# Optimization experiments

Hardware: AMD Instinct MI355X
Metric: run time of the kernel (lower is better)

## Reference

```python
import jax, jax.numpy as jnp
import numpy as np
import math

B, T, C = 2, 1024, 1024
NEMBD = 1024
NATTN = 1024
NHEAD = 16
CTX = 1024
HS = NATTN // NHEAD          # head size = 64
ROT = HS // 2                # rotary dims = 32


def rotate_half(x):
    x1, x2 = x[..., : x.shape[-1] // 2], x[..., x.shape[-1] // 2 :]
    return jnp.concatenate((-x2, x1), axis=-1)


def setup_inputs() -> dict:
    key = jax.random.key(0)
    ks = jax.random.split(key, 16)
    s = 0.02
    inp = {
        "x": jax.random.normal(ks[0], (B, T, C), dtype=jnp.float32),
        # time-decay params (torch inits them to ones; add noise for a nontrivial test)
        "time_w": 1.0 + s * jax.random.normal(ks[1], (NHEAD, CTX), dtype=jnp.float32),
        "time_alpha": 1.0 + s * jax.random.normal(ks[2], (NHEAD, 1, CTX), dtype=jnp.float32),
        "time_beta": 1.0 + s * jax.random.normal(ks[3], (NHEAD, CTX, 1), dtype=jnp.float32),
        "time_gamma": 1.0 + s * jax.random.normal(ks[4], (CTX, 1), dtype=jnp.float32),
        # projections (stored as (in, out) for x @ W)
        "Wq": s * jax.random.normal(ks[5], (NEMBD, NATTN), dtype=jnp.float32),
        "bq": s * jax.random.normal(ks[6], (NATTN,), dtype=jnp.float32),
        "Wk": s * jax.random.normal(ks[7], (NEMBD, NATTN), dtype=jnp.float32),
        "bk": s * jax.random.normal(ks[8], (NATTN,), dtype=jnp.float32),
        "Wv": s * jax.random.normal(ks[9], (NEMBD, NATTN), dtype=jnp.float32),
        "bv": s * jax.random.normal(ks[10], (NATTN,), dtype=jnp.float32),
        # 1x1 conv over head channels: (out_head, in_head)
        "Wmix": s * jax.random.normal(ks[11], (NHEAD, NHEAD), dtype=jnp.float32),
        "Wo": s * jax.random.normal(ks[12], (NATTN, NEMBD), dtype=jnp.float32),
        "bo": s * jax.random.normal(ks[13], (NEMBD,), dtype=jnp.float32),
    }
    return inp


def reference(x, time_w, time_alpha, time_beta, time_gamma,
              Wq, bq, Wk, bk, Wv, bv, Wmix, Wo, bo):
    Bx, Tx, Cx = x.shape
    TT = CTX

    # --- relative time-decay weight matrix (H, T, T) ---
    w = jnp.pad(time_w, ((0, 0), (0, TT)))          # (H, 2TT)
    w = jnp.tile(w, (1, TT))                        # (H, 2TT*TT)
    w = w[:, :-TT].reshape(NHEAD, TT, 2 * TT - 1)
    w = w[:, :, TT - 1:]                            # (H, TT, TT)
    w = w[:, :Tx, :Tx] * time_alpha[:, :, :Tx] * time_beta[:, :Tx, :]

    # --- time shift of the first half of channels ---
    half = Cx // 2
    x_shift = jnp.pad(x[:, :, :half], ((0, 0), (1, 0), (0, 0)))[:, :Tx, :]
    xs = jnp.concatenate([x_shift, x[:, :, half:]], axis=-1)

    # --- q/k/v projections -> (B, H, T, hs) ---
    q = (xs @ Wq + bq).reshape(Bx, Tx, NHEAD, HS).transpose(0, 2, 1, 3)
    k = (xs @ Wk + bk).reshape(Bx, Tx, NHEAD, HS).transpose(0, 2, 1, 3)
    v = (xs @ Wv + bv).reshape(Bx, Tx, NHEAD, HS).transpose(0, 2, 1, 3)

    # --- rotary on the first ROT dims of each head (base = ctx_len) ---
    qr, q_pass = q[..., :ROT], q[..., ROT:]
    kr, k_pass = k[..., :ROT], k[..., ROT:]
    inv_freq = 1.0 / (jnp.float32(CTX) ** (jnp.arange(0, ROT, 2, dtype=jnp.float32) / ROT))
    t = jnp.arange(Tx, dtype=jnp.float32)
    freqs = t[:, None] * inv_freq[None, :]          # (T, ROT/2)
    emb = jnp.concatenate((freqs, freqs), axis=-1)  # (T, ROT)
    cos, sin = jnp.cos(emb), jnp.sin(emb)
    qr = qr * cos + rotate_half(qr) * sin
    kr = kr * cos + rotate_half(kr) * sin
    q = jnp.concatenate((qr, q_pass), axis=-1)
    k = jnp.concatenate((kr, k_pass), axis=-1)

    # --- attention with time decay and cross-head 1x1 mix ---
    att = jnp.einsum('bhtd,bhsd->bhts', q, k) * (1.0 / math.sqrt(HS))
    att = jax.nn.softmax(att, axis=-1)
    att = att * w[None]                              # (B,H,T,T) * (1,H,T,T)
    att = jnp.einsum('gh,bhts->bgts', Wmix, att)     # 1x1 conv over head channel
    y = jnp.einsum('bhts,bhsd->bhtd', att, v)
    y = y.transpose(0, 2, 1, 3).reshape(Bx, Tx, NATTN)
    return (y @ Wo + bo) * time_gamma[:Tx, :]
```

## Files before the change

### kernel.cpp

```cpp
#include <hip/hip_runtime.h>

typedef unsigned short u16;
typedef unsigned int u32;
typedef __attribute__((ext_vector_type(8))) short bf16x8;
typedef __attribute__((ext_vector_type(4))) float f32x4;

#define MFMA(a,b,c) __builtin_amdgcn_mfma_f32_16x16x32_bf16(a,b,c,0,0,0)

__device__ __forceinline__ float b2f(u16 u){
  union { unsigned int i; float f; } v; v.i = ((unsigned int)u)<<16; return v.f;
}
__device__ __forceinline__ u16 f2b(float f){
  union { float f; unsigned int i; } v; v.f = f;
  unsigned int r = (v.i + 0x7FFFu + ((v.i>>16)&1u))>>16;
  return (u16)r;
}
__device__ __forceinline__ void gld16(const u16* g, u16* l){
  __builtin_amdgcn_global_load_lds((const __attribute__((address_space(1))) u32*)g,
                                   (__attribute__((address_space(3))) u32*)l, 16, 0, 0);
}

__global__ __launch_bounds__(256) void k_pre(
    const float* __restrict__ x,
    const float* __restrict__ Wq, const float* __restrict__ Wk,
    const float* __restrict__ Wv, const float* __restrict__ Wo,
    u16* __restrict__ xs, u16* __restrict__ WT, u16* __restrict__ WoT)
{
  int bid = blockIdx.x;
  int tid = threadIdx.x;
  if (bid < 1024){
    int idx = bid*256 + tid;
    size_t e = (size_t)idx*8;
    int c = (int)(e & 1023);
    int t = (int)((e>>10)&1023);
    float4 f0 = {0.f,0.f,0.f,0.f}, f1 = {0.f,0.f,0.f,0.f};
    const float* src = nullptr;
    if (c < 512){ if (t > 0) src = x + e - 1024; }
    else        { src = x + e; }
    if (src){ f0 = *(const float4*)src; f1 = *(const float4*)(src+4); }
    u16 o[8];
    o[0]=f2b(f0.x); o[1]=f2b(f0.y); o[2]=f2b(f0.z); o[3]=f2b(f0.w);
    o[4]=f2b(f1.x); o[5]=f2b(f1.y); o[6]=f2b(f1.z); o[7]=f2b(f1.w);
    *(uint4*)(xs + e) = *(const uint4*)o;
    return;
  }
  int z  = (bid-1024)>>8;
  int rc = (bid-1024)&255;
  const float* src = (z==0)?Wq:((z==1)?Wk:((z==2)?Wv:Wo));
  u16* dst = (z==3)? WoT : (WT + (size_t)z*1048576);
  int c0 = (rc&15)*64, r0 = (rc>>4)*64;
  __shared__ u16 tile[64][72];
  int r = tid>>2, cc = (tid&3)*16;
  const float* sp = src + (size_t)(r0+r)*1024 + c0+cc;
  float4 a0 = *(const float4*)(sp);
  float4 a1 = *(const float4*)(sp+4);
  float4 a2 = *(const float4*)(sp+8);
  float4 a3 = *(const float4*)(sp+12);
  tile[r][cc+0]=f2b(a0.x); tile[r][cc+1]=f2b(a0.y); tile[r][cc+2]=f2b(a0.z); tile[r][cc+3]=f2b(a0.w);
  tile[r][cc+4]=f2b(a1.x); tile[r][cc+5]=f2b(a1.y); tile[r][cc+6]=f2b(a1.z); tile[r][cc+7]=f2b(a1.w);
  tile[r][cc+8]=f2b(a2.x); tile[r][cc+9]=f2b(a2.y); tile[r][cc+10]=f2b(a2.z); tile[r][cc+11]=f2b(a2.w);
  tile[r][cc+12]=f2b(a3.x); tile[r][cc+13]=f2b(a3.y); tile[r][cc+14]=f2b(a3.z); tile[r][cc+15]=f2b(a3.w);
  __syncthreads();
  int c = tid>>2, rr = (tid&3)*16;
  uint4 o0,o1; u16* p0=(u16*)&o0; u16* p1=(u16*)&o1;
  #pragma unroll
  for (int i=0;i<8;i++){ p0[i]=tile[rr+i][c]; p1[i]=tile[rr+8+i][c]; }
  *(uint4*)(dst + (size_t)(c0+c)*1024 + r0+rr)   = o0;
  *(uint4*)(dst + (size_t)(c0+c)*1024 + r0+rr+8) = o1;
}

__global__ __launch_bounds__(256) void k_gemm_qkv(
    const u16* __restrict__ A, const u16* __restrict__ Bt,
    const float* __restrict__ bq, const float* __restrict__ bk, const float* __restrict__ bv,
    u16* __restrict__ qb, u16* __restrict__ kb, u16* __restrict__ vT)
{
  __shared__ u16 As[128*32];
  __shared__ u16 Bs[64*32];
  const int n0 = blockIdx.x*64, m0 = blockIdx.y*128;
  const int tid = threadIdx.x, lane = tid&63, wave = tid>>6;
  const int quad = lane>>4, l16 = lane&15;
  const int wm = (wave>>1)*64, wn = (wave&1)*32;
  f32x4 zero = {0.f,0.f,0.f,0.f};
  f32x4 acc[4][2];
  #pragma unroll
  for (int i=0;i<4;i++){ acc[i][0]=zero; acc[i][1]=zero; }
  const int srow = (lane>>2), scol = (lane&3)*8;
  const u16* pa0 = A  + (size_t)(m0 + wave*16 + srow)*1024 + scol;
  const u16* pb0 = Bt + (size_t)(n0 + wave*16 + srow)*1024 + scol;
  u16* lA0 = &As[(wave*16)*32];
  u16* lA1 = &As[(64 + wave*16)*32];
  u16* lB0 = &Bs[(wave*16)*32];
  for (int k0=0;k0<1024;k0+=32){
    __syncthreads();
    gld16(pa0 + k0,           lA0);
    gld16(pa0 + 64*1024 + k0, lA1);
    gld16(pb0 + k0,           lB0);
    __syncthreads();
    bf16x8 af[4], bfr[2];
    #pragma unroll
    for (int mt=0;mt<4;mt++) af[mt]  = *(const bf16x8*)&As[(wm+mt*16+l16)*32 + quad*8];
    #pragma unroll
    for (int nt=0;nt<2;nt++) bfr[nt] = *(const bf16x8*)&Bs[(wn+nt*16+l16)*32 + quad*8];
    #pragma unroll
    for (int mt=0;mt<4;mt++){
      acc[mt][0] = MFMA(af[mt], bfr[0], acc[mt][0]);
      acc[mt][1] = MFMA(af[mt], bfr[1], acc[mt][1]);
    }
  }
  const int which = n0>>10;
  const int nn0 = (n0 & 1023) + wn;
  const int h = (n0 & 1023)>>6;
  const float* barr = (which==0)?bq:((which==1)?bk:bv);
  float bias0 = barr[nn0 + l16];
  float bias1 = barr[nn0 + 16 + l16];
  if (which == 2){
    #pragma unroll
    for (int mt=0;mt<4;mt++)
      #pragma unroll
      for (int r=0;r<4;r++){
        int m = m0 + wm + mt*16 + quad*4 + r;
        int bb = m>>10, t = m&1023;
        size_t base = (size_t)(bb*16+h)*65536 + t;
        int d0 = wn + l16;
        vT[base + (size_t)d0*1024]      = f2b(acc[mt][0][r] + bias0);
        vT[base + (size_t)(d0+16)*1024] = f2b(acc[mt][1][r] + bias1);
      }
  } else {
    const float scale = (which==0)?0.125f:1.0f;
    u16* dst = (which==0)? qb : kb;
    if (wn == 0){
      const float e = exp2f(-0.625f*(float)l16);
      #pragma unroll
      for (int mt=0;mt<4;mt++)
        #pragma unroll
        for (int r=0;r<4;r++){
          int m = m0 + wm + mt*16 + quad*4 + r;
          int bb = m>>10, t = m&1023;
          float f = (float)t * e;
          float cs = cosf(f), sn = sinf(f);
          float x0 = acc[mt][0][r] + bias0;
          float x1 = acc[mt][1][r] + bias1;
          float v0 = (x0*cs - x1*sn)*scale;
          float v1 = (x1*cs + x0*sn)*scale;
          size_t ob = (((size_t)(bb*16+h))*1024 + (size_t)t)*64 + l16;
          dst[ob]    = f2b(v0);
          dst[ob+16] = f2b(v1);
        }
    } else {
      #pragma unroll
      for (int mt=0;mt<4;mt++)
        #pragma unroll
        for (int r=0;r<4;r++){
          int m = m0 + wm + mt*16 + quad*4 + r;
          int bb = m>>10, t = m&1023;
          float v2 = (acc[mt][0][r] + bias0)*scale;
          float v3 = (acc[mt][1][r] + bias1)*scale;
          size_t ob = (((size_t)(bb*16+h))*1024 + (size_t)t)*64 + 32 + l16;
          dst[ob]    = f2b(v2);
          dst[ob+16] = f2b(v3);
        }
    }
  }
}

__global__ __launch_bounds__(256) void k_gemm_out(
    const u16* __restrict__ A, const u16* __restrict__ Bt,
    const float* __restrict__ bo, const float* __restrict__ gamma, float* __restrict__ out)
{
  __shared__ u16 As[64*32];
  __shared__ u16 Bs[64*32];
  const int n0 = blockIdx.x*64, m0 = blockIdx.y*64;
  const int tid = threadIdx.x, lane = tid&63, wave = tid>>6;
  const int quad = lane>>4, l16 = lane&15;
  const int wm = (wave>>1)*32, wn = (wave&1)*32;
  f32x4 zero = {0.f,0.f,0.f,0.f};
  f32x4 acc[2][2];
  #pragma unroll
  for (int i=0;i<2;i++){ acc[i][0]=zero; acc[i][1]=zero; }
  const int srow = (lane>>2), scol = (lane&3)*8;
  const u16* pa0 = A  + (size_t)(m0 + wave*16 + srow)*1024 + scol;
  const u16* pb0 = Bt + (size_t)(n0 + wave*16 + srow)*1024 + scol;
  u16* lA0 = &As[(wave*16)*32];
  u16* lB0 = &Bs[(wave*16)*32];
  for (int k0=0;k0<1024;k0+=32){
    __syncthreads();
    gld16(pa0 + k0, lA0);
    gld16(pb0 + k0, lB0);
    __syncthreads();
    bf16x8 af[2], bfr[2];
    #pragma unroll
    for (int mt=0;mt<2;mt++) af[mt]  = *(const bf16x8*)&As[(wm+mt*16+l16)*32 + quad*8];
    #pragma unroll
    for (int nt=0;nt<2;nt++) bfr[nt] = *(const bf16x8*)&Bs[(wn+nt*16+l16)*32 + quad*8];
    #pragma unroll
    for (int mt=0;mt<2;mt++){
      acc[mt][0] = MFMA(af[mt], bfr[0], acc[mt][0]);
      acc[mt][1] = MFMA(af[mt], bfr[1], acc[mt][1]);
    }
  }
  #pragma unroll
  for (int nt=0;nt<2;nt++){
    int colg = n0 + wn + nt*16 + l16;
    float bias = bo[colg];
    #pragma unroll
    for (int mt=0;mt<2;mt++)
      #pragma unroll
      for (int r=0;r<4;r++){
        int m = m0 + wm + mt*16 + quad*4 + r;
        int t = m&1023;
        float val = (acc[mt][nt][r] + bias)*gamma[t];
        out[(size_t)m*1024 + colg] = val;
      }
  }
}

__global__ __launch_bounds__(1024) void k_sm(
    const u16* __restrict__ q, const u16* __restrict__ k,
    const float* __restrict__ tw, const float* __restrict__ alpha, const float* __restrict__ beta,
    u16* __restrict__ P)
{
  const int tb = blockIdx.x, h = blockIdx.y, b = blockIdx.z;
  const int t0b = tb*64;
  const int tid = threadIdx.x;
  const int wave = tid>>6, lane = tid&63, quad = lane>>4, l16 = lane&15;
  const int wt = wave>>2, ws = wave&3;

  __shared__ u16 qs[64*76];
  __shared__ u16 ks[256*76];
  __shared__ float tws[1024];
  __shared__ float als[1024];
  __shared__ float pm[4][64];
  __shared__ float pl[4][64];
  __shared__ float fm[64];
  __shared__ float fr[64];

  const size_t bh = (size_t)(b*16+h)*65536;
  const u16* qp = q + bh;
  const u16* kp = k + bh;

  if (tid < 512){
    int row = tid>>3, g = tid&7;
    *(uint4*)&qs[row*76 + g*8] = *(const uint4*)(qp + (size_t)(t0b+row)*64 + g*8);
  }
  tws[tid] = tw[h*1024 + tid];
  als[tid] = alpha[h*1024 + tid];
  __syncthreads();

  bf16x8 qf0 = *(const bf16x8*)&qs[(wt*16+l16)*76 + quad*8];
  bf16x8 qf1 = *(const bf16x8*)&qs[(wt*16+l16)*76 + quad*8 + 32];

  f32x4 acc[16];
  #pragma unroll
  for (int i=0;i<16;i++){ acc[i][0]=0.f; acc[i][1]=0.f; acc[i][2]=0.f; acc[i][3]=0.f; }

  #pragma unroll
  for (int c=0;c<4;c++){
    if (c) __syncthreads();
    {
      int row = tid>>3, g = tid&7;
      *(uint4*)&ks[row*76 + g*8]       = *(const uint4*)(kp + (size_t)(c*256+row)*64 + g*8);
      *(uint4*)&ks[(row+128)*76 + g*8] = *(const uint4*)(kp + (size_t)(c*256+row+128)*64 + g*8);
    }
    __syncthreads();
    #pragma unroll
    for (int j=0;j<4;j++){
      int lt = j*4 + ws;
      bf16x8 kf0 = *(const bf16x8*)&ks[(lt*16+l16)*76 + quad*8];
      bf16x8 kf1 = *(const bf16x8*)&ks[(lt*16+l16)*76 + quad*8 + 32];
      acc[c*4+j] = MFMA(qf0, kf0, acc[c*4+j]);
      acc[c*4+j] = MFMA(qf1, kf1, acc[c*4+j]);
    }
  }

  float mrow[4], lrow[4];
  #pragma unroll
  for (int r=0;r<4;r++){
    float m = acc[0][r];
    #pragma unroll
    for (int a=1;a<16;a++) m = fmaxf(m, acc[a][r]);
    #pragma unroll
    for (int off=1; off<16; off<<=1) m = fmaxf(m, __shfl_xor(m, off));
    float l = 0.f;
    #pragma unroll
    for (int a=0;a<16;a++) l += __expf(acc[a][r]-m);
    #pragma unroll
    for (int off=1; off<16; off<<=1) l += __shfl_xor(l, off);
    mrow[r]=m; lrow[r]=l;
  }
  if (l16==0){
    #pragma unroll
    for (int r=0;r<4;r++){
      pm[ws][wt*16+quad*4+r] = mrow[r];
      pl[ws][wt*16+quad*4+r] = lrow[r];
    }
  }
  __syncthreads();
  if (tid < 64){
    float m0s = pm[0][tid], m1s = pm[1][tid], m2s = pm[2][tid], m3s = pm[3][tid];
    float m = fmaxf(fmaxf(m0s,m1s), fmaxf(m2s,m3s));
    float l = pl[0][tid]*__expf(m0s-m) + pl[1][tid]*__expf(m1s-m)
            + pl[2][tid]*__expf(m2s-m) + pl[3][tid]*__expf(m3s-m);
    fm[tid] = m;
    fr[tid] = beta[h*1024 + t0b + tid] / l;
  }
  __syncthreads();

  u16* Pp = P + (((size_t)b)<<24) + (((size_t)h)<<10);
  float m_f[4], r_f[4]; int trow[4];
  #pragma unroll
  for (int r=0;r<4;r++){
    int rg = wt*16+quad*4+r;
    m_f[r] = fm[rg]; r_f[r] = fr[rg]; trow[r] = t0b + rg;
  }
  const int slim = tb*4 + wt;
  #pragma unroll
  for (int c=0;c<4;c++)
    #pragma unroll
    for (int j=0;j<4;j++){
      int st = c*16 + j*4 + ws;
      if (st > slim) continue;
      int s = st*16 + l16;
      float av = als[s];
      #pragma unroll
      for (int r=0;r<4;r++){
        int t = trow[r];
        float p = 0.f;
        if (s <= t)
          p = __expf(acc[c*4+j][r]-m_f[r])*r_f[r]*tws[1023+s-t]*av;
        Pp[((size_t)t<<14) + s] = f2b(p);
      }
    }
}

__global__ __launch_bounds__(256) void k_mix(const u16* __restrict__ P, const float* __restrict__ Wm,
                                             u16* __restrict__ Ab)
{
  const int t = blockIdx.x, b = blockIdx.y;
  const int tid = threadIdx.x;
  const int g = tid>>4, sg = tid&15;
  __shared__ u16 Ps[16*264];
  float w[16];
  #pragma unroll
  for (int h=0;h<16;h++) w[h] = Wm[g*16+h];
  const int tmaxr = t|15;
  const int ncw = (t>>8) + 1;
  const size_t slab = (((size_t)b)<<24) + (((size_t)t)<<14);
  const u16* pp = P + slab;
  u16* ap = Ab + slab;
  for (int c=0;c<ncw;c++){
    int s0 = c*256;
    if (c) __syncthreads();
    int colg = sg*16;
    uint4 z = {0u,0u,0u,0u};
    uint4 v0 = z, v1 = z;
    if (s0+colg <= tmaxr){
      v0 = *(const uint4*)(pp + ((size_t)g<<10) + s0+colg);
      v1 = *(const uint4*)(pp + ((size_t)g<<10) + s0+colg+8);
    }
    *(uint4*)&Ps[g*264+colg]   = v0;
    *(uint4*)&Ps[g*264+colg+8] = v1;
    __syncthreads();
    if (s0 + sg*16 > tmaxr) continue;
    float acc[16];
    #pragma unroll
    for (int i=0;i<16;i++) acc[i]=0.f;
    #pragma unroll
    for (int h=0;h<16;h++){
      float wh = w[h];
      #pragma unroll
      for (int j=0;j<4;j++){
        ushort4 u = *(const ushort4*)&Ps[h*264 + sg*16 + j*4];
        acc[j*4+0] += wh*b2f(u.x);
        acc[j*4+1] += wh*b2f(u.y);
        acc[j*4+2] += wh*b2f(u.z);
        acc[j*4+3] += wh*b2f(u.w);
      }
    }
    u16 o[16];
    #pragma unroll
    for (int i=0;i<16;i++) o[i] = f2b(acc[i]);
    *(uint4*)(ap + ((size_t)g<<10) + s0 + sg*16)     = *(uint4*)&o[0];
    *(uint4*)(ap + ((size_t)g<<10) + s0 + sg*16 + 8) = *(uint4*)&o[8];
  }
}

__global__ __launch_bounds__(1024) void k_pv(const u16* __restrict__ Ab, const u16* __restrict__ vT,
                                             u16* __restrict__ y)
{
  const int tb = blockIdx.x;
  const int bg = blockIdx.y;
  const int b = bg>>4, g = bg&15;
  const int t0b = tb*64;
  const int tid = threadIdx.x;
  const int wave = tid>>6, lane = tid&63, quad = lane>>4, l16 = lane&15;
  const int wt = wave>>2, wd = wave&3;
  __shared__ u16 As[64*264];
  __shared__ u16 Vs[64*264];
  const u16* ap = Ab + (((size_t)b)<<24) + ((size_t)g<<10);
  const u16* vp = vT + (size_t)bg*65536;
  f32x4 acc = {0.f,0.f,0.f,0.f};
  const int nc = tb/4 + 1;
  const int row = tid>>4, col = (tid&15)*16;
  const int trow_g = t0b + row;
  const int tmax = trow_g|15;
  for (int c=0;c<nc;c++){
    if (c) __syncthreads();
    int s0 = c*256;
    uint4 z = {0u,0u,0u,0u};
    uint4 a0 = z, a1 = z;
    if (s0 + col <= tmax){
      a0 = *(const uint4*)(ap + ((size_t)trow_g<<14) + s0+col);
      a1 = *(const uint4*)(ap + ((size_t)trow_g<<14) + s0+col+8);
    }
    *(uint4*)&As[row*264+col]   = a0;
    *(uint4*)&As[row*264+col+8] = a1;
    *(uint4*)&Vs[row*264+col]   = *(const uint4*)(vp + (size_t)row*1024 + s0+col);
    *(uint4*)&Vs[row*264+col+8] = *(const uint4*)(vp + (size_t)row*1024 + s0+col+8);
    __syncthreads();
    #pragma unroll
    for (int ks=0;ks<8;ks++){
      bf16x8 af  = *(const bf16x8*)&As[(wt*16+l16)*264 + ks*32 + quad*8];
      bf16x8 bfv = *(const bf16x8*)&Vs[(wd*16+l16)*264 + ks*32 + quad*8];
      acc = MFMA(af, bfv, acc);
    }
  }
  #pragma unroll
  for (int r=0;r<4;r++){
    int t = t0b + wt*16 + quad*4 + r;
    y[(size_t)(b*1024+t)*1024 + g*64 + wd*16 + l16] = f2b(acc[r]);
  }
}

__global__ void k_fail(float* out){ if (threadIdx.x==0) out[0] = 1e30f; }

extern "C" void kernel_launch(void* const* d_in, const int* in_sizes, int n_in,
                              void* d_out, int out_size, void* d_ws, size_t ws_size,
                              hipStream_t stream)
{
  const float* x     = (const float*)d_in[0];
  const float* tw    = (const float*)d_in[1];
  const float* alpha = (const float*)d_in[2];
  const float* beta  = (const float*)d_in[3];
  const float* gamma = (const float*)d_in[4];
  const float* Wq    = (const float*)d_in[5];
  const float* bq    = (const float*)d_in[6];
  const float* Wk    = (const float*)d_in[7];
  const float* bk    = (const float*)d_in[8];
  const float* Wv    = (const float*)d_in[9];
  const float* bv    = (const float*)d_in[10];
  const float* Wmix  = (const float*)d_in[11];
  const float* Wo    = (const float*)d_in[12];
  const float* bo    = (const float*)d_in[13];
  float* out = (float*)d_out;

  char* ws = (char*)d_ws;
  size_t off = 0;
  auto take = [&](size_t bytes)->char*{
    char* p = ws + off; off += (bytes + 255) & ~(size_t)255; return p;
  };
  u16*   xs  = (u16*)take((size_t)2097152*2);
  u16*   WT  = (u16*)take((size_t)3145728*2);
  u16*   WoT = (u16*)take((size_t)1048576*2);
  u16*   qb  = (u16*)take((size_t)2097152*2);
  u16*   kb  = (u16*)take((size_t)2097152*2);
  u16*   vTb = (u16*)take((size_t)2097152*2);
  u16*   yb  = (u16*)take((size_t)2097152*2);
  u16*   P   = (u16*)take((size_t)33554432*2);
  u16*   A   = (u16*)take((size_t)33554432*2);
  if (off > ws_size){
    hipLaunchKernelGGL(k_fail, dim3(1), dim3(64), 0, stream, out);
    return;
  }

  hipLaunchKernelGGL(k_pre, dim3(2048), dim3(256), 0, stream,
                     x, Wq, Wk, Wv, Wo, xs, WT, WoT);
  hipLaunchKernelGGL(k_gemm_qkv, dim3(48,16), dim3(256), 0, stream,
                     xs, WT, bq, bk, bv, qb, kb, vTb);
  hipLaunchKernelGGL(k_sm, dim3(16,16,2), dim3(1024), 0, stream,
                     qb, kb, tw, alpha, beta, P);
  hipLaunchKernelGGL(k_mix, dim3(1024,2), dim3(256), 0, stream, P, Wmix, A);
  hipLaunchKernelGGL(k_pv, dim3(16,32), dim3(1024), 0, stream, A, vTb, yb);
  hipLaunchKernelGGL(k_gemm_out, dim3(16,32), dim3(256), 0, stream, yb, WoT, bo, gamma, out);
}
```

Before: 208.3 us.

## Fuse cross-head mix into PV kernel and drop the intermediate mixed-attention buffer

Removes the separate k_mix kernel and the 64MB intermediate A buffer. The new k_mpv kernel computes the 16-head mix for each row chunk while staging the attention tile into LDS, then runs the PV MFMA loop as before. This eliminates a full write and re-read of the mixed attention matrix and one launch. The cost is that each output-head block now re-reads all 16 heads of P, so global or L2 read traffic for P rises up to 16x. The grid is reordered so that the 16 head blocks sharing a time tile are adjacent, which is meant to let those repeated reads hit in cache.

```diff
diff --git a/kernel.cpp b/kernel.cpp
--- a/kernel.cpp
+++ b/kernel.cpp
@@ -332,63 +332,11 @@
     }
 }
 
-__global__ __launch_bounds__(256) void k_mix(const u16* __restrict__ P, const float* __restrict__ Wm,
-                                             u16* __restrict__ Ab)
-{
-  const int t = blockIdx.x, b = blockIdx.y;
-  const int tid = threadIdx.x;
-  const int g = tid>>4, sg = tid&15;
-  __shared__ u16 Ps[16*264];
-  float w[16];
-  #pragma unroll
-  for (int h=0;h<16;h++) w[h] = Wm[g*16+h];
-  const int tmaxr = t|15;
-  const int ncw = (t>>8) + 1;
-  const size_t slab = (((size_t)b)<<24) + (((size_t)t)<<14);
-  const u16* pp = P + slab;
-  u16* ap = Ab + slab;
-  for (int c=0;c<ncw;c++){
-    int s0 = c*256;
-    if (c) __syncthreads();
-    int colg = sg*16;
-    uint4 z = {0u,0u,0u,0u};
-    uint4 v0 = z, v1 = z;
-    if (s0+colg <= tmaxr){
-      v0 = *(const uint4*)(pp + ((size_t)g<<10) + s0+colg);
-      v1 = *(const uint4*)(pp + ((size_t)g<<10) + s0+colg+8);
-    }
-    *(uint4*)&Ps[g*264+colg]   = v0;
-    *(uint4*)&Ps[g*264+colg+8] = v1;
-    __syncthreads();
-    if (s0 + sg*16 > tmaxr) continue;
-    float acc[16];
-    #pragma unroll
-    for (int i=0;i<16;i++) acc[i]=0.f;
-    #pragma unroll
-    for (int h=0;h<16;h++){
-      float wh = w[h];
-      #pragma unroll
-      for (int j=0;j<4;j++){
-        ushort4 u = *(const ushort4*)&Ps[h*264 + sg*16 + j*4];
-        acc[j*4+0] += wh*b2f(u.x);
-        acc[j*4+1] += wh*b2f(u.y);
-        acc[j*4+2] += wh*b2f(u.z);
-        acc[j*4+3] += wh*b2f(u.w);
-      }
-    }
-    u16 o[16];
-    #pragma unroll
-    for (int i=0;i<16;i++) o[i] = f2b(acc[i]);
-    *(uint4*)(ap + ((size_t)g<<10) + s0 + sg*16)     = *(uint4*)&o[0];
-    *(uint4*)(ap + ((size_t)g<<10) + s0 + sg*16 + 8) = *(uint4*)&o[8];
-  }
-}
-
-__global__ __launch_bounds__(1024) void k_pv(const u16* __restrict__ Ab, const u16* __restrict__ vT,
-                                             u16* __restrict__ y)
-{
-  const int tb = blockIdx.x;
-  const int bg = blockIdx.y;
+__global__ __launch_bounds__(1024) void k_mpv(const u16* __restrict__ P, const float* __restrict__ Wm,
+                                              const u16* __restrict__ vT, u16* __restrict__ y)
+{
+  const int bg = blockIdx.x;
+  const int tb = blockIdx.y;
   const int b = bg>>4, g = bg&15;
   const int t0b = tb*64;
   const int tid = threadIdx.x;
@@ -396,24 +344,44 @@
   const int wt = wave>>2, wd = wave&3;
   __shared__ u16 As[64*264];
   __shared__ u16 Vs[64*264];
-  const u16* ap = Ab + (((size_t)b)<<24) + ((size_t)g<<10);
+  float w[16];
+  #pragma unroll
+  for (int hh=0;hh<16;hh++) w[hh] = Wm[g*16+hh];
+  const u16* pp = P + (((size_t)b)<<24);
   const u16* vp = vT + (size_t)bg*65536;
   f32x4 acc = {0.f,0.f,0.f,0.f};
   const int nc = tb/4 + 1;
   const int row = tid>>4, col = (tid&15)*16;
-  const int trow_g = t0b + row;
-  const int tmax = trow_g|15;
+  const int tglob = t0b + row;
+  const int tmax = tglob|15;
+  const u16* prow = pp + ((size_t)tglob<<14);
   for (int c=0;c<nc;c++){
     if (c) __syncthreads();
     int s0 = c*256;
-    uint4 z = {0u,0u,0u,0u};
-    uint4 a0 = z, a1 = z;
+    float a[16];
+    #pragma unroll
+    for (int i=0;i<16;i++) a[i]=0.f;
     if (s0 + col <= tmax){
-      a0 = *(const uint4*)(ap + ((size_t)trow_g<<14) + s0+col);
-      a1 = *(const uint4*)(ap + ((size_t)trow_g<<14) + s0+col+8);
-    }
-    *(uint4*)&As[row*264+col]   = a0;
-    *(uint4*)&As[row*264+col+8] = a1;
+      #pragma unroll
+      for (int hh=0;hh<16;hh++){
+        const u16* qq = prow + (hh<<10) + s0 + col;
+        uint4 r0 = *(const uint4*)qq;
+        uint4 r1 = *(const uint4*)(qq+8);
+        float wh = w[hh];
+        const u16* p0 = (const u16*)&r0;
+        const u16* p1 = (const u16*)&r1;
+        #pragma unroll
+        for (int i=0;i<8;i++){
+          a[i]   += wh*b2f(p0[i]);
+          a[8+i] += wh*b2f(p1[i]);
+        }
+      }
+    }
+    u16 o[16];
+    #pragma unroll
+    for (int i=0;i<16;i++) o[i] = f2b(a[i]);
+    *(uint4*)&As[row*264+col]   = *(uint4*)&o[0];
+    *(uint4*)&As[row*264+col+8] = *(uint4*)&o[8];
     *(uint4*)&Vs[row*264+col]   = *(const uint4*)(vp + (size_t)row*1024 + s0+col);
     *(uint4*)&Vs[row*264+col+8] = *(const uint4*)(vp + (size_t)row*1024 + s0+col+8);
     __syncthreads();
@@ -466,7 +434,6 @@
   u16*   vTb = (u16*)take((size_t)2097152*2);
   u16*   yb  = (u16*)take((size_t)2097152*2);
   u16*   P   = (u16*)take((size_t)33554432*2);
-  u16*   A   = (u16*)take((size_t)33554432*2);
   if (off > ws_size){
     hipLaunchKernelGGL(k_fail, dim3(1), dim3(64), 0, stream, out);
     return;
@@ -478,7 +445,6 @@
                      xs, WT, bq, bk, bv, qb, kb, vTb);
   hipLaunchKernelGGL(k_sm, dim3(16,16,2), dim3(1024), 0, stream,
                      qb, kb, tw, alpha, beta, P);
-  hipLaunchKernelGGL(k_mix, dim3(1024,2), dim3(256), 0, stream, P, Wmix, A);
-  hipLaunchKernelGGL(k_pv, dim3(16,32), dim3(1024), 0, stream, A, vTb, yb);
+  hipLaunchKernelGGL(k_mpv, dim3(32,16), dim3(1024), 0, stream, P, Wmix, vTb, yb);
   hipLaunchKernelGGL(k_gemm_out, dim3(16,32), dim3(256), 0, stream, yb, WoT, bo, gamma, out);
 }
```

After: 248.8 us. 1.19x slower.
